# Kernel tuning notes

Hardware: AMD Instinct MI355X
Metric: run time of the kernel (lower is better)

## Reference

```python
import jax, jax.numpy as jnp
import numpy as np

EPS = 1e-5
CONV_CFG = [(10, 5, 3), (8, 5, 2), (4, 2, 1), (3, 1, 1), (3, 1, 1)]  # (kernel, stride, pad)


def conv_bn_relu(x, w, gamma, beta, stride, pad):
    # x: [B, Cin, L], w: [Cout, Cin, K]; BatchNorm1d in training mode (batch stats)
    y = jax.lax.conv_general_dilated(x, w, (stride,), [(pad, pad)],
                                     dimension_numbers=('NCH', 'OIH', 'NCH'))
    mean = y.mean(axis=(0, 2), keepdims=True)
    var = y.var(axis=(0, 2), keepdims=True)
    y = (y - mean) * jax.lax.rsqrt(var + EPS)
    return jax.nn.relu(y * gamma[None, :, None] + beta[None, :, None])


def encoder(x, ws, bn_gamma, bn_beta):
    for i, (k, s, p) in enumerate(CONV_CFG):
        x = conv_bn_relu(x, ws[i], bn_gamma[i], bn_beta[i], s, p)
    return x


def gru(seq, h0, wih, whh, bih, bhh):
    # seq: [B, T, D], h0: [B, H]. torch GRU gate order: r, z, n.
    x_proj = jnp.einsum('btd,gd->btg', seq, wih) + bih  # [B, T, 3H]

    def step(h, xp):
        hp = h @ whh.T + bhh
        xr, xz, xn = jnp.split(xp, 3, axis=-1)
        hr, hz, hn = jnp.split(hp, 3, axis=-1)
        r = jax.nn.sigmoid(xr + hr)
        zg = jax.nn.sigmoid(xz + hz)
        n = jnp.tanh(xn + r * hn)
        h_new = (1.0 - zg) * n + zg * h
        return h_new, h_new

    h_last, outs = jax.lax.scan(step, h0, jnp.swapaxes(x_proj, 0, 1))
    return jnp.swapaxes(outs, 0, 1), h_last


def setup_inputs() -> dict:
    key = jax.random.key(0)
    ks = jax.random.split(key, 16)
    B, L, T = 64, 20480, 12
    x = jax.random.normal(ks[0], (B, 1, L), dtype=jnp.float32)
    hidden = jnp.zeros((1, B, 256), dtype=jnp.float32)
    shapes = [(512, 1, 10), (512, 512, 8), (512, 512, 4), (512, 512, 3), (512, 512, 3)]
    ws = {}
    for i, sh in enumerate(shapes):
        fan_out = sh[0] * sh[2]
        ws['w%d' % (i + 1)] = jax.random.normal(ks[1 + i], sh, dtype=jnp.float32) * np.float32(np.sqrt(2.0 / fan_out))
    bn_gamma = jnp.ones((5, 512), dtype=jnp.float32)
    bn_beta = jnp.zeros((5, 512), dtype=jnp.float32)
    gru_wih = jax.random.normal(ks[6], (768, 512), dtype=jnp.float32) * np.float32(np.sqrt(2.0 / 768.0))
    gru_whh = jax.random.normal(ks[7], (768, 256), dtype=jnp.float32) * np.float32(np.sqrt(2.0 / 768.0))
    gru_bih = jnp.zeros((768,), dtype=jnp.float32)
    gru_bhh = jnp.zeros((768,), dtype=jnp.float32)
    wk_w = jax.random.normal(ks[8], (T, 512, 256), dtype=jnp.float32) * np.float32(np.sqrt(2.0 / 512.0))
    wk_b = jnp.zeros((T, 512), dtype=jnp.float32)
    inp = dict(x=x, hidden=hidden, bn_gamma=bn_gamma, bn_beta=bn_beta,
               gru_wih=gru_wih, gru_whh=gru_whh, gru_bih=gru_bih, gru_bhh=gru_bhh,
               wk_w=wk_w, wk_b=wk_b, t_samples=200)
    inp.update(ws)
    return inp


def reference(x, hidden, w1, w2, w3, w4, w5, bn_gamma, bn_beta,
              gru_wih, gru_whh, gru_bih, gru_bhh, wk_w, wk_b, t_samples):
    B = x.shape[0]
    T = wk_w.shape[0]
    t = int(t_samples)
    z = encoder(x, (w1, w2, w3, w4, w5), bn_gamma, bn_beta)  # [B, 512, Lz]
    z = jnp.swapaxes(z, 1, 2)                                # [B, Lz, 512]
    encode_samples = jnp.swapaxes(z[:, t + 1:t + 1 + T, :], 0, 1)  # [T, B, 512]
    forward_seq = z[:, :t + 1, :]
    output, h_last = gru(forward_seq, hidden[0], gru_wih, gru_whh, gru_bih, gru_bhh)
    c_t = output[:, t, :]                                    # [B, 256]
    pred = jnp.einsum('bd,tkd->tbk', c_t, wk_w) + wk_b[:, None, :]  # [T, B, 512]
    total = jnp.einsum('tbk,tck->tbc', encode_samples, pred)        # [T, B, B]
    logsm = jax.nn.log_softmax(total, axis=-1)  # nn.LogSoftmax() on 2D -> dim=1
    nce = jnp.sum(jnp.diagonal(logsm, axis1=1, axis2=2)) / (-1.0 * B * T)
    # torch overwrites `correct` each iteration -> final value is from the last timestep
    correct = jnp.sum(jnp.argmax(jax.nn.softmax(total[-1], axis=-1), axis=0) == jnp.arange(B))
    accuracy = correct.astype(jnp.float32) / B
    return accuracy, nce, h_last[None]
```

## Files before the change

kernel.cpp:

```cpp
#include <hip/hip_runtime.h>
#include <hip/hip_bf16.h>

typedef __hip_bfloat16 bf16;
typedef short short8v __attribute__((ext_vector_type(8)));
typedef float float4v __attribute__((ext_vector_type(4)));

__device__ __forceinline__ float ld_f(const float* p, size_t i) { return p[i]; }
__device__ __forceinline__ float ld_f(const bf16* p, size_t i) { return __bfloat162float(p[i]); }
__device__ __forceinline__ float bfb_to_f(short u) {
    return __uint_as_float(((unsigned int)(unsigned short)u) << 16);
}
__device__ __forceinline__ short f_to_bf16bits(float v) {
    bf16 h = __float2bfloat16(v);
    short s; __builtin_memcpy(&s, &h, 2); return s;
}
__device__ __forceinline__ unsigned int bn_pair(unsigned int u, float sc, float sh) {
    float x0 = bfb_to_f((short)(u & 0xffffu));
    float x1 = bfb_to_f((short)(u >> 16));
    float y0 = fmaxf(fmaf(sc, x0, sh), 0.0f);
    float y1 = fmaxf(fmaf(sc, x1, sh), 0.0f);
    return (unsigned int)(unsigned short)f_to_bf16bits(y0) |
           ((unsigned int)(unsigned short)f_to_bf16bits(y1) << 16);
}
__device__ __forceinline__ float sigmoidf_(float x) { return 1.0f / (1.0f + expf(-x)); }
// ... 14 lines not shown
    float v = (t < KW) ? w[((size_t)co * CIN + ci) * KW + t] : 0.0f;
    out[idx] = f_to_bf16bits(v);
}

__global__ __launch_bounds__(256) void pack_gruw(const float* __restrict__ whh, short* __restrict__ wfrag) {
    int idx = blockIdx.x * 256 + threadIdx.x;
    if (idx >= 196608) return;
    int j = idx & 7;
    int lane = (idx >> 3) & 63;
    int f = idx >> 9;
    int wv = f / 48;
    int r = f - wv * 48;
    int mt = r >> 3, kc = r & 7;
    int m = lane & 15, quad = lane >> 4;
    int row = (wv * 6 + mt) * 16 + m;
    int col = kc * 32 + quad * 8 + j;
    wfrag[idx] = f_to_bf16bits(whh[(size_t)row * 256 + col]);
}

__global__ __launch_bounds__(256) void pack_all(const float* __restrict__ w3, const float* __restrict__ w4,
                                                const float* __restrict__ w5, const float* __restrict__ wih,
                                                const float* __restrict__ whh,
                                                short* __restrict__ o3, short* __restrict__ o4,
                                                short* __restrict__ o5, short* __restrict__ owih,
                                                short* __restrict__ ogru) {
    int idx = blockIdx.x * 256 + threadIdx.x;
    const int NC = 512 * 512 * 4;
    if (idx < NC) {
        int co = idx >> 11, r = idx & 2047;
        int ci = r >> 2, t = r & 3;
        o3[idx] = f_to_bf16bits(w3[((size_t)co * 512 + ci) * 4 + t]);
        return;
    }
    idx -= NC;
    if (idx < NC) {
        int co = idx >> 11, r = idx & 2047;
        int ci = r >> 2, t = r & 3;
        o4[idx] = (t < 3) ? f_to_bf16bits(w4[((size_t)co * 512 + ci) * 3 + t]) : 0;
        return;
    }
    idx -= NC;
    if (idx < NC) {
        int co = idx >> 11, r = idx & 2047;
        int ci = r >> 2, t = r & 3;
        o5[idx] = (t < 3) ? f_to_bf16bits(w5[((size_t)co * 512 + ci) * 3 + t]) : 0;
        return;
    }
    idx -= NC;
    if (idx < 393216) {
        owih[idx] = f_to_bf16bits(wih[idx]);
        return;
    }
    idx -= 393216;
    if (idx < 196608) {
        int j = idx & 7;
        int lane = (idx >> 3) & 63;
        int f = idx >> 9;
        int wv = f / 48;
        int r = f - wv * 48;
        int mt = r >> 3, kc = r & 7;
        int m = lane & 15, quad = lane >> 4;
        int row = (wv * 6 + mt) * 16 + m;
        int col = kc * 32 + quad * 8 + j;
        ogru[idx] = f_to_bf16bits(whh[(size_t)row * 256 + col]);
    }
}

__global__ __launch_bounds__(256) void bn_fin(const float* __restrict__ sums, const float* __restrict__ gamma,
                                              const float* __restrict__ beta, int layer, float invM,
                                              float* __restrict__ ss) {
    int c = blockIdx.x * 256 + threadIdx.x;
    if (c >= 512) return;
    float mean = sums[c] * invM;
    float var = sums[512 + c] * invM - mean * mean;
    float sc = rsqrtf(var + 1e-5f) * gamma[layer * 512 + c];
    ss[c] = sc;
    ss[512 + c] = beta[layer * 512 + c] - mean * sc;
}

template <int KWP, int ST, int SPANP, bool BNIN, bool STATS>
__global__ __launch_bounds__(256, 3) void conv_mfma6(const bf16* __restrict__ in,
                                                     const short* __restrict__ wpk,
                                                     bf16* __restrict__ out,
                                                     int Lin, int Lout, int pad,
                                                     const float* __restrict__ ssin,
                                                     float* __restrict__ sums_out) {
    constexpr int KTOT = 512 * KWP;
    constexpr int NCHUNK = KTOT / 32;
    constexpr int CCC = 32 / KWP;
    constexpr int W16 = SPANP / 8;
    constexpr int NU = CCC * W16;
    constexpr int NLD = (NU + 255) / 256;

    const int l0 = blockIdx.x * 128;
    const int co0 = blockIdx.y * 128;
    const int tid = threadIdx.x;
    const int lane = tid & 63;
    const int wv = tid >> 6;
    const int m = lane & 15;
    const int quad = lane >> 4;
    const int nh = wv * 32;

    in += (size_t)blockIdx.z * 512 * Lin;
    out += (size_t)blockIdx.z * 512 * Lout;
    const short* ins = (const short*)in;

    __shared__ __align__(16) short As[2][128][40];
    __shared__ __align__(16) short rows[2][CCC][SPANP];
    __shared__ float bsum[STATS ? 128 : 1][2];

    const int base = ST * l0 - pad;
    const int g0a = base & ~7;
    const int off = base - g0a;

    const int arow = tid >> 2, aseg = tid & 3;

    float4v acc[8][2];
#pragma unroll
    for (int i = 0; i < 8; ++i) { acc[i][0] = (float4v){0,0,0,0}; acc[i][1] = (float4v){0,0,0,0}; }

    uint4 pa0, pa1;
    uint4 rbuf[NLD];

    auto load_stage = [&](int kc) {
        const int k0 = kc * 32;
        const int ci0 = kc * CCC;
        pa0 = *(const uint4*)(wpk + (size_t)(co0 + arow) * KTOT + k0 + aseg * 8);
        pa1 = *(const uint4*)(wpk + (size_t)(co0 + arow + 64) * KTOT + k0 + aseg * 8);
#pragma unroll
        for (int r = 0; r < NLD; ++r) {
            int e = tid + r * 256;
            if (NU % 256 == 0 || e < NU) {
                int cc = e / W16, col = e - cc * W16;
                int gs = g0a + col * 8;
                const short* src = ins + (size_t)(ci0 + cc) * Lin;
                if (gs >= 0 && gs + 8 <= Lin) {
                    rbuf[r] = *(const uint4*)(src + gs);
                } else {
                    float sc = 0.f, sh = 0.f;
                    if constexpr (BNIN) { sc = ssin[ci0 + cc]; sh = ssin[512 + ci0 + cc]; }
                    unsigned short tmp[8];
#pragma unroll
                    for (int j = 0; j < 8; ++j) {
                        int g = gs + j;
                        float xv = 0.f;
                        if (g >= 0 && g < Lin) {
                            xv = bfb_to_f(src[g]);
                            if constexpr (BNIN) xv = fmaxf(fmaf(sc, xv, sh), 0.0f);
                        }
                        tmp[j] = (unsigned short)f_to_bf16bits(xv);
                    }
                    uint4 v;
                    v.x = tmp[0] | ((unsigned int)tmp[1] << 16);
                    v.y = tmp[2] | ((unsigned int)tmp[3] << 16);
                    v.z = tmp[4] | ((unsigned int)tmp[5] << 16);
                    v.w = tmp[6] | ((unsigned int)tmp[7] << 16);
                    rbuf[r] = v;
                }
            }
        }
    };
    auto commit = [&](int buf, int kc) {
        *(uint4*)&As[buf][arow][aseg * 8] = pa0;
        *(uint4*)&As[buf][arow + 64][aseg * 8] = pa1;
        const int ci0 = kc * CCC;
#pragma unroll
        for (int r = 0; r < NLD; ++r) {
            int e = tid + r * 256;
            if (NU % 256 == 0 || e < NU) {
                int cc = e / W16, col = e - cc * W16;
                uint4 v = rbuf[r];
                if constexpr (BNIN) {
                    int gs = g0a + col * 8;
                    if (gs >= 0 && gs + 8 <= Lin) {
                        float sc = ssin[ci0 + cc], sh = ssin[512 + ci0 + cc];
                        v.x = bn_pair(v.x, sc, sh);
                        v.y = bn_pair(v.y, sc, sh);
                        v.z = bn_pair(v.z, sc, sh);
                        v.w = bn_pair(v.w, sc, sh);
                    }
                }
                *(uint4*)&rows[buf][cc][col * 8] = v;
            }
        }
    };

    if (STATS && tid < 128) { bsum[tid][0] = 0.f; bsum[tid][1] = 0.f; }
// ... 7 lines not shown

        short8v afrag[8], bfrag[2];
#pragma unroll
        for (int s = 0; s < 8; ++s)
            afrag[s] = *(const short8v*)&As[cur][s * 16 + m][quad * 8];
#pragma unroll
        for (int t = 0; t < 2; ++t) {
            const int ll = nh + t * 16 + m;
            short8v bf;
            if constexpr (KWP == 8) {
                const short* rp = &rows[cur][quad][off + ST * ll];
#pragma unroll
                for (int j = 0; j < 8; ++j) bf[j] = rp[j];
            } else {
                const short* ra = &rows[cur][quad * 2 + 0][off + ST * ll];
                const short* rb = &rows[cur][quad * 2 + 1][off + ST * ll];
#pragma unroll
                for (int j = 0; j < 4; ++j) { bf[j] = ra[j]; bf[4 + j] = rb[j]; }
            }
            bfrag[t] = bf;
        }
#pragma unroll
        for (int s = 0; s < 8; ++s)
#pragma unroll
            for (int t = 0; t < 2; ++t)
                acc[s][t] = __builtin_amdgcn_mfma_f32_16x16x32_bf16(afrag[s], bfrag[t], acc[s][t], 0, 0, 0);

        if (kc + 1 < NCHUNK) commit(cur ^ 1, kc + 1);
        __syncthreads();
    }

    const bool v0 = (l0 + nh + m) < Lout;
    const bool v1 = (l0 + nh + 16 + m) < Lout;
#pragma unroll
    for (int t = 0; t < 2; ++t) {
        const int l = l0 + nh + t * 16 + m;
        if (t ? v1 : v0) {
#pragma unroll
            for (int s = 0; s < 8; ++s) {
#pragma unroll
                for (int reg = 0; reg < 4; ++reg) {
                    const int co = co0 + s * 16 + quad * 4 + reg;
                    out[(size_t)co * Lout + l] = __float2bfloat16(acc[s][t][reg]);
                }
            }
        }
    }

    if constexpr (STATS) {
#pragma unroll
        for (int s = 0; s < 8; ++s) {
            float p1[4], p2[4];
#pragma unroll
            for (int reg = 0; reg < 4; ++reg) {
                float a0 = v0 ? acc[s][0][reg] : 0.f;
                float a1 = v1 ? acc[s][1][reg] : 0.f;
                p1[reg] = a0 + a1;
                p2[reg] = a0 * a0 + a1 * a1;
            }
#pragma unroll
            for (int o = 1; o <= 8; o <<= 1) {
#pragma unroll
                for (int reg = 0; reg < 4; ++reg) {
                    p1[reg] += __shfl_xor(p1[reg], o);
                    p2[reg] += __shfl_xor(p2[reg], o);
                }
            }
            if (m == 0) {
#pragma unroll
                for (int reg = 0; reg < 4; ++reg) {
                    atomicAdd(&bsum[s * 16 + quad * 4 + reg][0], p1[reg]);
                    atomicAdd(&bsum[s * 16 + quad * 4 + reg][1], p2[reg]);
                }
            }
        }
        __syncthreads();
        if (tid < 128) {
            atomicAdd(&sums_out[co0 + tid], bsum[tid][0]);
            atomicAdd(&sums_out[512 + co0 + tid], bsum[tid][1]);
        }
    }
}

__global__ __launch_bounds__(256) void conv1_mfma(const float* __restrict__ x,
                                                  const short* __restrict__ w1p,
                                                  const float* __restrict__ ss,
                                                  bf16* __restrict__ y1c, int nbase) {
    const int l0 = blockIdx.x * 64;
    const int co0 = blockIdx.y * 128;
    const int nloc = blockIdx.z;
    const int n = nbase + nloc;
    const int tid = threadIdx.x;
    const int lane = tid & 63;
    const int wv = tid >> 6;
    const int m = lane & 15;
    const int quad = lane >> 4;

    __shared__ __align__(16) short xs[352];
    const int base = 5 * l0 - 3;
    for (int e = tid; e < 347; e += 256) {
        int g = base + e;
        float v = (g >= 0 && g < 20480) ? x[(size_t)n * 20480 + g] : 0.0f;
        xs[e] = f_to_bf16bits(v);
    }
    __syncthreads();

    const int lloc = wv * 16 + m;
    short8v bfrag;
    {
        const short* rp = &xs[5 * lloc + quad * 8];
#pragma unroll
        for (int j = 0; j < 8; ++j) bfrag[j] = rp[j];
    }
    float4v acc[8];
#pragma unroll
    for (int s = 0; s < 8; ++s) {
        short8v afrag = *(const short8v*)(w1p + (size_t)(co0 + s * 16 + m) * 32 + quad * 8);
        float4v z = (float4v){0.f, 0.f, 0.f, 0.f};
        acc[s] = __builtin_amdgcn_mfma_f32_16x16x32_bf16(afrag, bfrag, z, 0, 0, 0);
    }
    const int l = l0 + lloc;
#pragma unroll
    for (int s = 0; s < 8; ++s) {
#pragma unroll
        for (int reg = 0; reg < 4; ++reg) {
            const int co = co0 + s * 16 + quad * 4 + reg;
            float v = fmaxf(acc[s][reg] * ss[co] + ss[512 + co], 0.0f);
            y1c[((size_t)nloc * 512 + co) * 4096 + l] = __float2bfloat16(v);
        }
    }
}

__global__ __launch_bounds__(256) void conv1_stats(const float* __restrict__ x,
                                                   const float* __restrict__ w1,
                                                   float* __restrict__ sums) {
    const int n = blockIdx.x;
    const int tid = threadIdx.x;
    __shared__ __align__(16) float ws[5120];
    __shared__ __align__(16) float xs[5 * 256 + 10];
    for (int e = tid; e < 5120; e += 256) ws[e] = w1[e];
    const int co0 = tid, co1 = tid + 256;
    float a1_0 = 0.0f, a2_0 = 0.0f, a1_1 = 0.0f, a2_1 = 0.0f;
    for (int i = 0; i < 4; ++i) {
        const int c = blockIdx.y * 4 + i;
        const int base = c * 1280 - 3;
        __syncthreads();
        for (int e = tid; e < 1290; e += 256) {
            int g = base + e;
            xs[e] = (g >= 0 && g < 20480) ? x[(size_t)n * 20480 + g] : 0.0f;
        }
        __syncthreads();
        for (int l = 0; l < 256; ++l) {
            float y0 = 0.0f, y1v = 0.0f;
#pragma unroll
            for (int t = 0; t < 10; ++t) {
                float xv = xs[5 * l + t];
                y0 += ws[co0 * 10 + t] * xv;
                y1v += ws[co1 * 10 + t] * xv;
            }
            a1_0 += y0; a2_0 += y0 * y0;
            a1_1 += y1v; a2_1 += y1v * y1v;
        }
    }
    atomicAdd(&sums[co0], a1_0); atomicAdd(&sums[512 + co0], a2_0);
    atomicAdd(&sums[co1], a1_1); atomicAdd(&sums[512 + co1], a2_1);
}

__global__ __launch_bounds__(256) void bn1_finalize(const float* __restrict__ sums,
                                                    const float* __restrict__ gamma,
                                                    const float* __restrict__ beta,
                                                    float* __restrict__ ss) {
    int c = blockIdx.x * 256 + threadIdx.x;
    if (c >= 512) return;
    const float invM = 1.0f / (64.0f * 4096.0f);
    float mean = sums[c] * invM;
    float var = sums[512 + c] * invM - mean * mean;
    float sc = rsqrtf(var + 1e-5f) * gamma[c];
    ss[c] = sc;
    ss[512 + c] = beta[c] - mean * sc;
}

__global__ __launch_bounds__(256) void bn_stats_v(const bf16* __restrict__ y, float* __restrict__ sums, int L) {
    const int c = blockIdx.x, n = blockIdx.y;
    const short* p = (const short*)y + ((size_t)n * 512 + c) * L;
    float s1 = 0.f, s2 = 0.f;
    for (int l = threadIdx.x; l < L; l += 256) {
        float v = bfb_to_f(p[l]);
        s1 += v; s2 += v * v;
    }
#pragma unroll
    for (int off = 32; off > 0; off >>= 1) {
        s1 += __shfl_down(s1, off, 64);
        s2 += __shfl_down(s2, off, 64);
    }
    __shared__ float r1[4], r2[4];
    const int lane = threadIdx.x & 63, wv = threadIdx.x >> 6;
    if (lane == 0) { r1[wv] = s1; r2[wv] = s2; }
    __syncthreads();
    if (threadIdx.x == 0) {
        atomicAdd(&sums[c], r1[0] + r1[1] + r1[2] + r1[3]);
        atomicAdd(&sums[512 + c], r2[0] + r2[1] + r2[2] + r2[3]);
    }
}

__global__ __launch_bounds__(256) void bn_apply_v(bf16* __restrict__ y, const float* __restrict__ sums,
                                                  const float* __restrict__ gamma, const float* __restrict__ beta,
                                                  int layer, int L) {
    const int c = blockIdx.x, n = blockIdx.y;
    const float invM = 1.0f / (64.0f * (float)L);
    float mean = sums[c] * invM;
    float var = sums[512 + c] * invM - mean * mean;
    float sc = rsqrtf(var + 1e-5f) * gamma[layer * 512 + c];
    float sh = beta[layer * 512 + c] - mean * sc;
    short* p = (short*)y + ((size_t)n * 512 + c) * L;
    for (int l = threadIdx.x; l < L; l += 256) {
        float v = bfb_to_f(p[l]);
        p[l] = f_to_bf16bits(fmaxf(v * sc + sh, 0.0f));
    }
}

__global__ __launch_bounds__(256) void xproj_mfma(const bf16* __restrict__ y5,
                                                  const short* __restrict__ wihp,
                                                  const float* __restrict__ bih,
                                                  float* __restrict__ xp,
                                                  const int* __restrict__ tsamp) {
    const int t0 = blockIdx.x * 64;
    const int g0 = blockIdx.y * 128;
    const int b = blockIdx.z;
    const int tid = threadIdx.x;
    const int lane = tid & 63;
    const int wv = tid >> 6;
    const int m = lane & 15;
    const int quad = lane >> 4;
    const int ts = tsamp[0];

    __shared__ __align__(16) short As[128][40];
    __shared__ __align__(16) short Bt[32][66];

    float4v acc[8];
#pragma unroll
    for (int i = 0; i < 8; ++i) acc[i] = (float4v){0.f, 0.f, 0.f, 0.f};

    const short* y5s = (const short*)y5;
    for (int kc = 0; kc < 16; ++kc) {
        const int k0 = kc * 32;
        __syncthreads();
#pragma unroll
        for (int r = 0; r < 2; ++r) {
            int e = tid + r * 256;
            int row = e >> 2, seg = e & 3;
            *(uint4*)&As[row][seg * 8] =
                *(const uint4*)(wihp + (size_t)(g0 + row) * 512 + k0 + seg * 8);
        }
        for (int e = tid; e < 2048; e += 256) {
            int cc = e >> 6, tl = e & 63;
            Bt[cc][tl] = y5s[((size_t)b * 512 + k0 + cc) * 409 + t0 + tl];
        }
        __syncthreads();
        short8v bfrag;
#pragma unroll
        for (int j = 0; j < 8; ++j) bfrag[j] = Bt[quad * 8 + j][wv * 16 + m];
#pragma unroll
        for (int s = 0; s < 8; ++s) {
            short8v afrag = *(const short8v*)&As[s * 16 + m][quad * 8];
            acc[s] = __builtin_amdgcn_mfma_f32_16x16x32_bf16(afrag, bfrag, acc[s], 0, 0, 0);
        }
    }
    const int t = t0 + wv * 16 + m;
    if (t <= ts) {
#pragma unroll
        for (int s = 0; s < 8; ++s) {
#pragma unroll
            for (int reg = 0; reg < 4; ++reg) {
                const int g = g0 + s * 16 + quad * 4 + reg;
                xp[((size_t)b * 256 + t) * 768 + g] = acc[s][reg] + bih[g];
            }
        }
    }
}

__global__ __launch_bounds__(512, 2) void gru_mfma(const float* __restrict__ xproj,
                                                   const short* __restrict__ wfrag,
                                                   const float* __restrict__ hidden,
                                                   const float* __restrict__ bhh,
                                                   float* __restrict__ hlast,
                                                   const int* __restrict__ tsamp) {
    const int b = blockIdx.x;
    const int tid = threadIdx.x;
    const int lane = tid & 63;
    const int wv = tid >> 6;
    const int m = lane & 15;
    const int quad = lane >> 4;

    __shared__ float hf[256];
    __shared__ __align__(16) short hbs[256];
    __shared__ float pre[768];

    short8v wreg[48];
    {
        const short* wb = wfrag + ((size_t)(wv * 48) * 64 + lane) * 8;
#pragma unroll
        for (int f = 0; f < 48; ++f) wreg[f] = *(const short8v*)(wb + (size_t)f * 512);
    }
    if (wv < 4) {
        float hv = hidden[(size_t)b * 256 + tid];
        hf[tid] = hv;
        hbs[tid] = f_to_bf16bits(hv);
    }
    const int ts = tsamp[0];
    const float* xb = xproj + (size_t)b * 256 * 768;
    float bhr = 0.f, bhz = 0.f, bhn = 0.f, nxr = 0.f, nxz = 0.f, nxn = 0.f;
    if (wv < 4) {
        bhr = bhh[tid]; bhz = bhh[256 + tid]; bhn = bhh[512 + tid];
        nxr = xb[tid]; nxz = xb[256 + tid]; nxn = xb[512 + tid];
    }

    for (int step = 0; step <= ts; ++step) {
        __syncthreads();
        float4v acc[6];
#pragma unroll
        for (int i = 0; i < 6; ++i) acc[i] = (float4v){0.f, 0.f, 0.f, 0.f};
#pragma unroll
        for (int kc = 0; kc < 8; ++kc) {
            short8v bfrag = *(const short8v*)&hbs[kc * 32 + quad * 8];
#pragma unroll
            for (int mt = 0; mt < 6; ++mt)
                acc[mt] = __builtin_amdgcn_mfma_f32_16x16x32_bf16(wreg[mt * 8 + kc], bfrag, acc[mt], 0, 0, 0);
        }
        if (m == 0) {
#pragma unroll
            for (int mt = 0; mt < 6; ++mt)
#pragma unroll
                for (int reg = 0; reg < 4; ++reg)
                    pre[wv * 96 + mt * 16 + quad * 4 + reg] = acc[mt][reg];
        }
        __syncthreads();
        if (wv < 4) {
            const int g = tid;
            float r = sigmoidf_(nxr + bhr + pre[g]);
            float z = sigmoidf_(nxz + bhz + pre[256 + g]);
            float nn = tanhf(nxn + r * (bhn + pre[512 + g]));
            float hnew = (1.0f - z) * nn + z * hf[g];
            hf[g] = hnew;
            hbs[g] = f_to_bf16bits(hnew);
            if (step < ts) {
                const float* xs = xb + (size_t)(step + 1) * 768;
                nxr = xs[g]; nxz = xs[256 + g]; nxn = xs[512 + g];
            }
        }
    }
    __syncthreads();
    if (wv < 4) hlast[(size_t)b * 256 + tid] = hf[tid];
}

__global__ __launch_bounds__(256) void pred_kernel(const float* __restrict__ hlast, const float* __restrict__ wkw,
                                                   const float* __restrict__ wkb, float* __restrict__ pred) {
    const int c = blockIdx.x, t = blockIdx.y;
    __shared__ __align__(16) float hs[256];
    hs[threadIdx.x] = hlast[(size_t)c * 256 + threadIdx.x];
    __syncthreads();
    for (int k = threadIdx.x; k < 512; k += 256) {
        const float* wr = wkw + ((size_t)t * 512 + k) * 256;
        float acc = 0.0f;
        for (int d = 0; d < 256; d += 4) {
            float4 w4 = *(const float4*)&wr[d];
            acc += w4.x * hs[d] + w4.y * hs[d + 1] + w4.z * hs[d + 2] + w4.w * hs[d + 3];
        }
        pred[((size_t)t * 64 + c) * 512 + k] = acc + wkb[(size_t)t * 512 + k];
    }
}

__global__ __launch_bounds__(64) void total_kernel(const bf16* __restrict__ y5, const float* __restrict__ pred,
                                                   float* __restrict__ total, const int* __restrict__ tsamp) {
    const int b = blockIdx.x, t = blockIdx.y;
    const int col = tsamp[0] + 1 + t;
    __shared__ __align__(16) float es[512];
    for (int k = threadIdx.x; k < 512; k += 64) es[k] = ld_f(y5, ((size_t)b * 512 + k) * 409 + col);
    __syncthreads();
    const int c = threadIdx.x;
    const float* pr = pred + ((size_t)t * 64 + c) * 512;
    float acc = 0.0f;
    for (int k = 0; k < 512; k += 4) {
        float4 p4 = *(const float4*)&pr[k];
        acc += p4.x * es[k] + p4.y * es[k + 1] + p4.z * es[k + 2] + p4.w * es[k + 3];
    }
    total[((size_t)t * 64 + b) * 64 + c] = acc;
}

__global__ __launch_bounds__(256) void final_kernel(const float* __restrict__ total, const float* __restrict__ hlast,
                                                    float* __restrict__ out) {
    __shared__ float rowM[768], rowS[768];
    __shared__ float red[256];
    __shared__ int cnt[64];
    const int tid = threadIdx.x;
    float local = 0.0f;
    for (int row = tid; row < 768; row += 256) {
        const float* r = total + (size_t)row * 64;
        float m = r[0];
        for (int c = 1; c < 64; ++c) m = fmaxf(m, r[c]);
        float s = 0.0f;
        for (int c = 0; c < 64; ++c) s += expf(r[c] - m);
        rowM[row] = m; rowS[row] = s;
        int bcol = row & 63;
        local += r[bcol] - m - logf(s);
    }
    red[tid] = local;
    __syncthreads();
    for (int o = 128; o > 0; o >>= 1) {
        if (tid < o) red[tid] += red[tid + o];
        __syncthreads();
    }
    if (tid == 0) out[1] = red[0] / (-768.0f);
    if (tid < 64) {
        const int c = tid;
        float best = -1e30f; int bi = -1;
        for (int b = 0; b < 64; ++b) {
            int row = 11 * 64 + b;
            float v = expf(total[(size_t)row * 64 + c] - rowM[row]) / rowS[row];
            if (v > best) { best = v; bi = b; }
        }
        cnt[c] = (bi == c) ? 1 : 0;
    }
    __syncthreads();
    if (tid == 0) {
        int s = 0;
        for (int c = 0; c < 64; ++c) s += cnt[c];
        out[0] = (float)s / 64.0f;
    }
    for (int i = tid; i < 16384; i += 256) out[2 + i] = hlast[i];
}

extern "C" void kernel_launch(void* const* d_in, const int* in_sizes, int n_in,
                              void* d_out, int out_size, void* d_ws, size_t ws_size,
                              hipStream_t stream) {
    const float *x = nullptr, *hidden = nullptr, *gamma = nullptr, *beta = nullptr;
    const float *wih = nullptr, *whh = nullptr, *bih = nullptr, *bhh = nullptr;
    const float *wkw = nullptr, *wkb = nullptr;
    const float *w1 = nullptr, *w2 = nullptr, *w3 = nullptr, *w4 = nullptr, *w5 = nullptr;
    const int* tsamp = nullptr;
    for (int i = 0; i < n_in; ++i) {
        const float* p = (const float*)d_in[i];
        switch (in_sizes[i]) {
            case 1310720: x = p; break;
            case 16384:   hidden = p; break;
            case 2560:    if (!gamma) gamma = p; else beta = p; break;
            case 393216:  wih = p; break;
            case 196608:  whh = p; break;
            case 768:     if (!bih) bih = p; else bhh = p; break;
            case 1572864: wkw = p; break;
            case 6144:    wkb = p; break;
            case 1:       tsamp = (const int*)d_in[i]; break;
            case 5120:    w1 = p; break;
            case 2097152: w2 = p; break;
            case 1048576: w3 = p; break;
            case 786432:  if (!w4) w4 = p; else w5 = p; break;
            default: break;
        }
    }

    char* ws = (char*)d_ws;
    const size_t SLOT_B = 57872384ull;
    int NBC = 8;
    if (ws_size >= SLOT_B + 64ull * 4194304ull + 81920ull) NBC = 64;
    else if (ws_size >= SLOT_B + 32ull * 4194304ull + 81920ull) NBC = 32;
    else if (ws_size >= SLOT_B + 16ull * 4194304ull + 81920ull) NBC = 16;

    bf16*  y2    = (bf16*)(ws + 0);
    bf16*  y4    = (bf16*)(ws + 0);
    float* xp    = (float*)(ws + 0);
    short* wconv = (short*)(ws + 53676032ull);
    bf16*  y1c   = (bf16*)(ws + SLOT_B);
    bf16*  y3    = (bf16*)(ws + SLOT_B);
    bf16*  y5    = (bf16*)(ws + SLOT_B);
    const size_t tail = SLOT_B + (size_t)NBC * 4194304ull;
    float* sums  = (float*)(ws + tail);
    float* ss1   = (float*)(ws + tail + 20480ull);
    float* ss2   = (float*)(ws + tail + 24576ull);
    float* ss3   = (float*)(ws + tail + 28672ull);
    float* ss4   = (float*)(ws + tail + 32768ull);
    short* w1p   = (short*)(ws + tail + 36864ull);

    float* hlast = (float*)(ws + 54855680ull);
    float* pred  = (float*)(ws + 54921216ull);
    float* totl  = (float*)(ws + 56494080ull);

    short *wpk3, *wpk4, *wpk5, *wihp, *wfrag;
    if (NBC == 64) {
        wpk3  = (short*)(ws + SLOT_B + 33554432ull);
        wpk4  = wpk3 + 1048576;
        wpk5  = wpk4 + 1048576;
        wihp  = wpk5 + 1048576;
        wfrag = wihp + 393216;
    } else {
        wpk3 = wpk4 = wpk5 = wconv;
        wihp  = (short*)(ws + 53676032ull);
        wfrag = (short*)(ws + 54462464ull);
    }

    zero_kernel<<<20, 256, 0, stream>>>(sums, 5120);
    conv1_stats<<<dim3(64, 4), 256, 0, stream>>>(x, w1, sums);
    bn1_finalize<<<2, 256, 0, stream>>>(sums, gamma, beta, ss1);
    pack_gemm<<<64, 256, 0, stream>>>(w1, w1p, 512, 1, 10, 32);
    pack_gemm<<<8192, 256, 0, stream>>>(w2, wconv, 512, 512, 8, 8);

    if (NBC == 64) {
        conv1_mfma<<<dim3(64, 4, 64), 256, 0, stream>>>(x, w1p, ss1, y1c, 0);
        conv_mfma6<8, 5, 656, false, true><<<dim3(7, 4, 64), 256, 0, stream>>>(
            y1c, wconv, y2, 4096, 819, 2, nullptr, sums + 1024);
        pack_all<<<14592, 256, 0, stream>>>(w3, w4, w5, wih, whh, wpk3, wpk4, wpk5, wihp, wfrag);
        bn_fin<<<2, 256, 0, stream>>>(sums + 1024, gamma, beta, 1, 1.0f / (64.0f * 819.0f), ss2);

        conv_mfma6<4, 2, 272, true, true><<<dim3(4, 4, 64), 256, 0, stream>>>(
            y2, wpk3, y3, 819, 409, 1, ss2, sums + 2048);
        bn_fin<<<2, 256, 0, stream>>>(sums + 2048, gamma, beta, 2, 1.0f / (64.0f * 409.0f), ss3);

        conv_mfma6<4, 1, 144, true, true><<<dim3(4, 4, 64), 256, 0, stream>>>(
            y3, wpk4, y4, 409, 409, 1, ss3, sums + 3072);
        bn_fin<<<2, 256, 0, stream>>>(sums + 3072, gamma, beta, 3, 1.0f / (64.0f * 409.0f), ss4);

        conv_mfma6<4, 1, 144, true, true><<<dim3(4, 4, 64), 256, 0, stream>>>(
            y4, wpk5, y5, 409, 409, 1, ss4, sums + 4096);
        bn_apply_v<<<dim3(512, 64), 256, 0, stream>>>(y5, sums + 4096, gamma, beta, 4, 409);
    } else {
        for (int nb = 0; nb < 64; nb += NBC) {
            conv1_mfma<<<dim3(64, 4, NBC), 256, 0, stream>>>(x, w1p, ss1, y1c, nb);
            conv_mfma6<8, 5, 656, false, false><<<dim3(7, 4, NBC), 256, 0, stream>>>(
                y1c, wconv, y2 + (size_t)nb * 512 * 819, 4096, 819, 2, nullptr, nullptr);
        }
        bn_stats_v<<<dim3(512, 64), 256, 0, stream>>>(y2, sums + 1024, 819);
        bn_apply_v<<<dim3(512, 64), 256, 0, stream>>>(y2, sums + 1024, gamma, beta, 1, 819);

        pack_gemm<<<4096, 256, 0, stream>>>(w3, wconv, 512, 512, 4, 4);
        conv_mfma6<4, 2, 272, false, false><<<dim3(4, 4, 64), 256, 0, stream>>>(
            y2, wconv, y3, 819, 409, 1, nullptr, nullptr);
        bn_stats_v<<<dim3(512, 64), 256, 0, stream>>>(y3, sums + 2048, 409);
        bn_apply_v<<<dim3(512, 64), 256, 0, stream>>>(y3, sums + 2048, gamma, beta, 2, 409);

        pack_gemm<<<4096, 256, 0, stream>>>(w4, wconv, 512, 512, 3, 4);
        conv_mfma6<4, 1, 144, false, false><<<dim3(4, 4, 64), 256, 0, stream>>>(
            y3, wconv, y4, 409, 409, 1, nullptr, nullptr);
        bn_stats_v<<<dim3(512, 64), 256, 0, stream>>>(y4, sums + 3072, 409);
        bn_apply_v<<<dim3(512, 64), 256, 0, stream>>>(y4, sums + 3072, gamma, beta, 3, 409);

        pack_gemm<<<4096, 256, 0, stream>>>(w5, wconv, 512, 512, 3, 4);
        conv_mfma6<4, 1, 144, false, false><<<dim3(4, 4, 64), 256, 0, stream>>>(
            y4, wconv, y5, 409, 409, 1, nullptr, nullptr);
        bn_stats_v<<<dim3(512, 64), 256, 0, stream>>>(y5, sums + 4096, 409);
        bn_apply_v<<<dim3(512, 64), 256, 0, stream>>>(y5, sums + 4096, gamma, beta, 4, 409);

        pack_gemm<<<1536, 256, 0, stream>>>(wih, wihp, 768, 512, 1, 1);
        pack_gruw<<<768, 256, 0, stream>>>(whh, wfrag);
    }

    xproj_mfma<<<dim3(4, 6, 64), 256, 0, stream>>>(y5, wihp, bih, xp, tsamp);
    gru_mfma<<<64, 512, 0, stream>>>(xp, wfrag, hidden, bhh, hlast, tsamp);

    pred_kernel<<<dim3(64, 12), 256, 0, stream>>>(hlast, wkw, wkb, pred);
    total_kernel<<<dim3(64, 12), 64, 0, stream>>>(y5, pred, totl, tsamp);
    final_kernel<<<1, 256, 0, stream>>>(totl, hlast, (float*)d_out);
}
```

Measured before the change: 2.120 ms.

## Add full-channel double-buffered conv kernel and fold final BN into consumers

Adds conv_mfma7, where each block covers all 512 output channels for a 64-column tile. It double-buffers the weight and input-row staging through registers and LDS, so each input row is read once rather than by four channel-blocks. Layers 3-5 now use it with a 7x64 grid. The standalone bn_apply pass over y5 is replaced by a small scale/shift finalize that xproj and total_kernel apply on load, removing a full read-modify-write of the activation. Risks: the larger LDS footprint and 128 accumulator registers per thread may limit occupancy, and a stray label was added before a launch.

```diff
diff --git a/kernel.cpp b/kernel.cpp
--- a/kernel.cpp
+++ b/kernel.cpp
@@ -314,6 +314,197 @@
     }
 }
 
+template <int KWP, int ST, int SPANP, bool BNIN, bool STATS>
+__global__ __launch_bounds__(256, 2) void conv_mfma7(const bf16* __restrict__ in,
+                                                     const short* __restrict__ wpk,
+                                                     bf16* __restrict__ out,
+                                                     int Lin, int Lout, int pad,
+                                                     const float* __restrict__ ssin,
+                                                     float* __restrict__ sums_out) {
+    constexpr int KTOT = 512 * KWP;
+    constexpr int NCHUNK = KTOT / 32;
+    constexpr int CCC = 32 / KWP;
+    constexpr int W16 = SPANP / 8;
+    constexpr int NU = CCC * W16;
+
+    const int l0 = blockIdx.x * 64;
+    const int tid = threadIdx.x;
+    const int lane = tid & 63;
+    const int wv = tid >> 6;
+    const int m = lane & 15;
+    const int quad = lane >> 4;
+    const int ch = (wv >> 1) * 256;
+    const int wl = (wv & 1) * 32;
+
+    in += (size_t)blockIdx.y * 512 * Lin;
+    out += (size_t)blockIdx.y * 512 * Lout;
+    const short* ins = (const short*)in;
+
+    __shared__ __align__(16) short As[2][512][32];
+    __shared__ __align__(16) short rows[2][CCC][SPANP];
+    __shared__ float bsum[STATS ? 512 : 1][2];
+
+    const int base = ST * l0 - pad;
+    const int g0a = base & ~7;
+    const int off = base - g0a;
+
+    const int aco = tid >> 2, aseg = tid & 3;
+
+    float4v acc[16][2];
+#pragma unroll
+    for (int i = 0; i < 16; ++i) { acc[i][0] = (float4v){0,0,0,0}; acc[i][1] = (float4v){0,0,0,0}; }
+
+    uint4 pa[8];
+    uint4 rb;
+
+    auto load_stage = [&](int kc) {
+        const int k0 = kc * 32;
+        const int ci0 = kc * CCC;
+#pragma unroll
+        for (int r = 0; r < 8; ++r)
+            pa[r] = *(const uint4*)(wpk + (size_t)(aco + r * 64) * KTOT + k0 + aseg * 8);
+        if (tid < NU) {
+            int cc = tid / W16, col = tid - cc * W16;
+            int gs = g0a + col * 8;
+            const short* src = ins + (size_t)(ci0 + cc) * Lin;
+            if (gs >= 0 && gs + 8 <= Lin) {
+                rb = *(const uint4*)(src + gs);
+            } else {
+                float sc = 0.f, sh = 0.f;
+                if constexpr (BNIN) { sc = ssin[ci0 + cc]; sh = ssin[512 + ci0 + cc]; }
+                unsigned short tmp[8];
+#pragma unroll
+                for (int j = 0; j < 8; ++j) {
+                    int g = gs + j;
+                    float xv = 0.f;
+                    if (g >= 0 && g < Lin) {
+                        xv = bfb_to_f(src[g]);
+                        if constexpr (BNIN) xv = fmaxf(fmaf(sc, xv, sh), 0.0f);
+                    }
+                    tmp[j] = (unsigned short)f_to_bf16bits(xv);
+                }
+                uint4 v;
+                v.x = tmp[0] | ((unsigned int)tmp[1] << 16);
+                v.y = tmp[2] | ((unsigned int)tmp[3] << 16);
+                v.z = tmp[4] | ((unsigned int)tmp[5] << 16);
+                v.w = tmp[6] | ((unsigned int)tmp[7] << 16);
+                rb = v;
+            }
+        }
+    };
+    auto commit = [&](int buf, int kc) {
+#pragma unroll
+        for (int r = 0; r < 8; ++r)
+            *(uint4*)&As[buf][aco + r * 64][aseg * 8] = pa[r];
+        if (tid < NU) {
+            int cc = tid / W16, col = tid - cc * W16;
+            uint4 v = rb;
+            if constexpr (BNIN) {
+                int gs = g0a + col * 8;
+                if (gs >= 0 && gs + 8 <= Lin) {
+                    const int ci0 = kc * CCC;
+                    float sc = ssin[ci0 + cc], sh = ssin[512 + ci0 + cc];
+                    v.x = bn_pair(v.x, sc, sh);
+                    v.y = bn_pair(v.y, sc, sh);
+                    v.z = bn_pair(v.z, sc, sh);
+                    v.w = bn_pair(v.w, sc, sh);
+                }
+            }
+            *(uint4*)&rows[buf][cc][col * 8] = v;
+        }
+    };
+
+    if (STATS) {
+        for (int i = tid; i < 512; i += 256) { bsum[i][0] = 0.f; bsum[i][1] = 0.f; }
+    }
+    load_stage(0);
+    commit(0, 0);
+    __syncthreads();
+
+    for (int kc = 0; kc < NCHUNK; ++kc) {
+        const int cur = kc & 1;
+        if (kc + 1 < NCHUNK) load_stage(kc + 1);
+
+        short8v bfrag[2];
+#pragma unroll
+        for (int t = 0; t < 2; ++t) {
+            const int ll = wl + t * 16 + m;
+            short8v bf;
+            if constexpr (KWP == 8) {
+                const short* rp = &rows[cur][quad][off + ST * ll];
+#pragma unroll
+                for (int j = 0; j < 8; ++j) bf[j] = rp[j];
+            } else {
+                const short* ra = &rows[cur][quad * 2 + 0][off + ST * ll];
+                const short* rb2 = &rows[cur][quad * 2 + 1][off + ST * ll];
+#pragma unroll
+                for (int j = 0; j < 4; ++j) { bf[j] = ra[j]; bf[4 + j] = rb2[j]; }
+            }
+            bfrag[t] = bf;
+        }
+#pragma unroll
+        for (int s = 0; s < 16; ++s) {
+            short8v afrag = *(const short8v*)&As[cur][ch + s * 16 + m][quad * 8];
+            acc[s][0] = __builtin_amdgcn_mfma_f32_16x16x32_bf16(afrag, bfrag[0], acc[s][0], 0, 0, 0);
+            acc[s][1] = __builtin_amdgcn_mfma_f32_16x16x32_bf16(afrag, bfrag[1], acc[s][1], 0, 0, 0);
+        }
+
+        if (kc + 1 < NCHUNK) commit(cur ^ 1, kc + 1);
+        __syncthreads();
+    }
+
+    const bool v0 = (l0 + wl + m) < Lout;
+    const bool v1 = (l0 + wl + 16 + m) < Lout;
+#pragma unroll
+    for (int t = 0; t < 2; ++t) {
+        const int l = l0 + wl + t * 16 + m;
+        if (t ? v1 : v0) {
+#pragma unroll
+            for (int s = 0; s < 16; ++s) {
+#pragma unroll
+                for (int reg = 0; reg < 4; ++reg) {
+                    const int co = ch + s * 16 + quad * 4 + reg;
+                    out[(size_t)co * Lout + l] = __float2bfloat16(acc[s][t][reg]);
+                }
+            }
+        }
+    }
+
+    if constexpr (STATS) {
+#pragma unroll
+        for (int s = 0; s < 16; ++s) {
+            float p1[4], p2[4];
+#pragma unroll
+            for (int reg = 0; reg < 4; ++reg) {
+                float a0 = v0 ? acc[s][0][reg] : 0.f;
+                float a1 = v1 ? acc[s][1][reg] : 0.f;
+                p1[reg] = a0 + a1;
+                p2[reg] = a0 * a0 + a1 * a1;
+            }
+#pragma unroll
+            for (int o = 1; o <= 8; o <<= 1) {
+#pragma unroll
+                for (int reg = 0; reg < 4; ++reg) {
+                    p1[reg] += __shfl_xor(p1[reg], o);
+                    p2[reg] += __shfl_xor(p2[reg], o);
+                }
+            }
+            if (m == 0) {
+#pragma unroll
+                for (int reg = 0; reg < 4; ++reg) {
+                    atomicAdd(&bsum[ch + s * 16 + quad * 4 + reg][0], p1[reg]);
+                    atomicAdd(&bsum[ch + s * 16 + quad * 4 + reg][1], p2[reg]);
+                }
+            }
+        }
+        __syncthreads();
+        for (int i = tid; i < 512; i += 256) {
+            atomicAdd(&sums_out[i], bsum[i][0]);
+            atomicAdd(&sums_out[512 + i], bsum[i][1]);
+        }
+    }
+}
+
 __global__ __launch_bounds__(256) void conv1_mfma(const float* __restrict__ x,
                                                   const short* __restrict__ w1p,
                                                   const float* __restrict__ ss,
@@ -398,20 +589,6 @@
     atomicAdd(&sums[co1], a1_1); atomicAdd(&sums[512 + co1], a2_1);
 }
 
-__global__ __launch_bounds__(256) void bn1_finalize(const float* __restrict__ sums,
-                                                    const float* __restrict__ gamma,
-                                                    const float* __restrict__ beta,
-                                                    float* __restrict__ ss) {
-    int c = blockIdx.x * 256 + threadIdx.x;
-    if (c >= 512) return;
-    const float invM = 1.0f / (64.0f * 4096.0f);
-    float mean = sums[c] * invM;
-    float var = sums[512 + c] * invM - mean * mean;
-    float sc = rsqrtf(var + 1e-5f) * gamma[c];
-    ss[c] = sc;
-    ss[512 + c] = beta[c] - mean * sc;
-}
-
 __global__ __launch_bounds__(256) void bn_stats_v(const bf16* __restrict__ y, float* __restrict__ sums, int L) {
     const int c = blockIdx.x, n = blockIdx.y;
     const short* p = (const short*)y + ((size_t)n * 512 + c) * L;
@@ -454,6 +631,7 @@
 __global__ __launch_bounds__(256) void xproj_mfma(const bf16* __restrict__ y5,
                                                   const short* __restrict__ wihp,
                                                   const float* __restrict__ bih,
+                                                  const float* __restrict__ ssy,
                                                   float* __restrict__ xp,
                                                   const int* __restrict__ tsamp) {
     const int t0 = blockIdx.x * 64;
@@ -486,7 +664,9 @@
         }
         for (int e = tid; e < 2048; e += 256) {
             int cc = e >> 6, tl = e & 63;
-            Bt[cc][tl] = y5s[((size_t)b * 512 + k0 + cc) * 409 + t0 + tl];
+            float sc = ssy[k0 + cc], sh = ssy[512 + k0 + cc];
+            float xv = bfb_to_f(y5s[((size_t)b * 512 + k0 + cc) * 409 + t0 + tl]);
+            Bt[cc][tl] = f_to_bf16bits(fmaxf(fmaf(sc, xv, sh), 0.0f));
         }
         __syncthreads();
         short8v bfrag;
@@ -603,11 +783,15 @@
 }
 
 __global__ __launch_bounds__(64) void total_kernel(const bf16* __restrict__ y5, const float* __restrict__ pred,
+                                                   const float* __restrict__ ssy,
                                                    float* __restrict__ total, const int* __restrict__ tsamp) {
     const int b = blockIdx.x, t = blockIdx.y;
     const int col = tsamp[0] + 1 + t;
     __shared__ __align__(16) float es[512];
-    for (int k = threadIdx.x; k < 512; k += 64) es[k] = ld_f(y5, ((size_t)b * 512 + k) * 409 + col);
+    for (int k = threadIdx.x; k < 512; k += 64) {
+        float xv = ld_f(y5, ((size_t)b * 512 + k) * 409 + col);
+        es[k] = fmaxf(fmaf(ssy[k], xv, ssy[512 + k]), 0.0f);
+    }
     __syncthreads();
     const int c = threadIdx.x;
     const float* pr = pred + ((size_t)t * 64 + c) * 512;
@@ -693,9 +877,9 @@
     char* ws = (char*)d_ws;
     const size_t SLOT_B = 57872384ull;
     int NBC = 8;
-    if (ws_size >= SLOT_B + 64ull * 4194304ull + 81920ull) NBC = 64;
-    else if (ws_size >= SLOT_B + 32ull * 4194304ull + 81920ull) NBC = 32;
-    else if (ws_size >= SLOT_B + 16ull * 4194304ull + 81920ull) NBC = 16;
+    if (ws_size >= SLOT_B + 64ull * 4194304ull + 98304ull) NBC = 64;
+    else if (ws_size >= SLOT_B + 32ull * 4194304ull + 98304ull) NBC = 32;
+    else if (ws_size >= SLOT_B + 16ull * 4194304ull + 98304ull) NBC = 16;
 
     bf16*  y2    = (bf16*)(ws + 0);
     bf16*  y4    = (bf16*)(ws + 0);
@@ -710,7 +894,8 @@
     float* ss2   = (float*)(ws + tail + 24576ull);
     float* ss3   = (float*)(ws + tail + 28672ull);
     float* ss4   = (float*)(ws + tail + 32768ull);
-    short* w1p   = (short*)(ws + tail + 36864ull);
+    float* ss5   = (float*)(ws + tail + 36864ull);
+    short* w1p   = (short*)(ws + tail + 40960ull);
 
     float* hlast = (float*)(ws + 54855680ull);
     float* pred  = (float*)(ws + 54921216ull);
@@ -731,7 +916,8 @@
 
     zero_kernel<<<20, 256, 0, stream>>>(sums, 5120);
     conv1_stats<<<dim3(64, 4), 256, 0, stream>>>(x, w1, sums);
-    bn1_finalize<<<2, 256, 0, stream>>>(sums, gamma, beta, ss1);
+    bn1_finalize_launch:
+    bn_fin<<<2, 256, 0, stream>>>(sums, gamma, beta, 0, 1.0f / (64.0f * 4096.0f), ss1);
     pack_gemm<<<64, 256, 0, stream>>>(w1, w1p, 512, 1, 10, 32);
     pack_gemm<<<8192, 256, 0, stream>>>(w2, wconv, 512, 512, 8, 8);
 
@@ -742,17 +928,17 @@
         pack_all<<<14592, 256, 0, stream>>>(w3, w4, w5, wih, whh, wpk3, wpk4, wpk5, wihp, wfrag);
         bn_fin<<<2, 256, 0, stream>>>(sums + 1024, gamma, beta, 1, 1.0f / (64.0f * 819.0f), ss2);
 
-        conv_mfma6<4, 2, 272, true, true><<<dim3(4, 4, 64), 256, 0, stream>>>(
+        conv_mfma7<4, 2, 144, true, true><<<dim3(7, 64), 256, 0, stream>>>(
             y2, wpk3, y3, 819, 409, 1, ss2, sums + 2048);
         bn_fin<<<2, 256, 0, stream>>>(sums + 2048, gamma, beta, 2, 1.0f / (64.0f * 409.0f), ss3);
 
-        conv_mfma6<4, 1, 144, true, true><<<dim3(4, 4, 64), 256, 0, stream>>>(
+        conv_mfma7<4, 1, 80, true, true><<<dim3(7, 64), 256, 0, stream>>>(
             y3, wpk4, y4, 409, 409, 1, ss3, sums + 3072);
         bn_fin<<<2, 256, 0, stream>>>(sums + 3072, gamma, beta, 3, 1.0f / (64.0f * 409.0f), ss4);
 
-        conv_mfma6<4, 1, 144, true, true><<<dim3(4, 4, 64), 256, 0, stream>>>(
+        conv_mfma7<4, 1, 80, true, true><<<dim3(7, 64), 256, 0, stream>>>(
             y4, wpk5, y5, 409, 409, 1, ss4, sums + 4096);
-        bn_apply_v<<<dim3(512, 64), 256, 0, stream>>>(y5, sums + 4096, gamma, beta, 4, 409);
+        bn_fin<<<2, 256, 0, stream>>>(sums + 4096, gamma, beta, 4, 1.0f / (64.0f * 409.0f), ss5);
     } else {
         for (int nb = 0; nb < 64; nb += NBC) {
             conv1_mfma<<<dim3(64, 4, NBC), 256, 0, stream>>>(x, w1p, ss1, y1c, nb);
@@ -763,31 +949,31 @@
         bn_apply_v<<<dim3(512, 64), 256, 0, stream>>>(y2, sums + 1024, gamma, beta, 1, 819);
 
         pack_gemm<<<4096, 256, 0, stream>>>(w3, wconv, 512, 512, 4, 4);
-        conv_mfma6<4, 2, 272, false, false><<<dim3(4, 4, 64), 256, 0, stream>>>(
+        conv_mfma7<4, 2, 144, false, false><<<dim3(7, 64), 256, 0, stream>>>(
             y2, wconv, y3, 819, 409, 1, nullptr, nullptr);
         bn_stats_v<<<dim3(512, 64), 256, 0, stream>>>(y3, sums + 2048, 409);
         bn_apply_v<<<dim3(512, 64), 256, 0, stream>>>(y3, sums + 2048, gamma, beta, 2, 409);
 
         pack_gemm<<<4096, 256, 0, stream>>>(w4, wconv, 512, 512, 3, 4);
-        conv_mfma6<4, 1, 144, false, false><<<dim3(4, 4, 64), 256, 0, stream>>>(
+        conv_mfma7<4, 1, 80, false, false><<<dim3(7, 64), 256, 0, stream>>>(
             y3, wconv, y4, 409, 409, 1, nullptr, nullptr);
         bn_stats_v<<<dim3(512, 64), 256, 0, stream>>>(y4, sums + 3072, 409);
         bn_apply_v<<<dim3(512, 64), 256, 0, stream>>>(y4, sums + 3072, gamma, beta, 3, 409);
 
         pack_gemm<<<4096, 256, 0, stream>>>(w5, wconv, 512, 512, 3, 4);
-        conv_mfma6<4, 1, 144, false, false><<<dim3(4, 4, 64), 256, 0, stream>>>(
+        conv_mfma7<4, 1, 80, false, false><<<dim3(7, 64), 256, 0, stream>>>(
             y4, wconv, y5, 409, 409, 1, nullptr, nullptr);
         bn_stats_v<<<dim3(512, 64), 256, 0, stream>>>(y5, sums + 4096, 409);
-        bn_apply_v<<<dim3(512, 64), 256, 0, stream>>>(y5, sums + 4096, gamma, beta, 4, 409);
+        bn_fin<<<2, 256, 0, stream>>>(sums + 4096, gamma, beta, 4, 1.0f / (64.0f * 409.0f), ss5);
 
         pack_gemm<<<1536, 256, 0, stream>>>(wih, wihp, 768, 512, 1, 1);
         pack_gruw<<<768, 256, 0, stream>>>(whh, wfrag);
     }
 
-    xproj_mfma<<<dim3(4, 6, 64), 256, 0, stream>>>(y5, wihp, bih, xp, tsamp);
+    xproj_mfma<<<dim3(4, 6, 64), 256, 0, stream>>>(y5, wihp, bih, ss5, xp, tsamp);
     gru_mfma<<<64, 512, 0, stream>>>(xp, wfrag, hidden, bhh, hlast, tsamp);
 
     pred_kernel<<<dim3(64, 12), 256, 0, stream>>>(hlast, wkw, wkb, pred);
-    total_kernel<<<dim3(64, 12), 64, 0, stream>>>(y5, pred, totl, tsamp);
+    total_kernel<<<dim3(64, 12), 64, 0, stream>>>(y5, pred, ss5, totl, tsamp);
     final_kernel<<<1, 256, 0, stream>>>(totl, hlast, (float*)d_out);
 }
```

New measurement: 2.528 ms. 1.19x slower.

## Fold final BN into consumers and swizzle conv block order for L2 reuse

Applied to the files above, without the earlier changes.

Drops the standalone bn_apply pass over y5 and instead computes scale/shift with bn_fin, applying BN+ReLU on the fly in xproj_mfma and total_kernel loads. This removes a full read-modify-write pass over the last activation tensor. Conv blocks now use a 1D grid remapped so that groups of 8 length tiles cycle through all 4 output-channel tiles consecutively, aiming for better cache reuse of input tiles. It also changes the workspace layout to add an ss5 slot.

```diff
diff --git a/kernel.cpp b/kernel.cpp
--- a/kernel.cpp
+++ b/kernel.cpp
@@ -120,7 +120,7 @@
 __global__ __launch_bounds__(256, 3) void conv_mfma6(const bf16* __restrict__ in,
                                                      const short* __restrict__ wpk,
                                                      bf16* __restrict__ out,
-                                                     int Lin, int Lout, int pad,
+                                                     int Lin, int Lout, int pad, int NL,
                                                      const float* __restrict__ ssin,
                                                      float* __restrict__ sums_out) {
     constexpr int KTOT = 512 * KWP;
@@ -130,8 +130,14 @@
     constexpr int NU = CCC * W16;
     constexpr int NLD = (NU + 255) / 256;
 
-    const int l0 = blockIdx.x * 128;
-    const int co0 = blockIdx.y * 128;
+    const int lin = blockIdx.x;
+    const int co_t = (lin >> 3) & 3;
+    const int u = ((lin >> 5) << 3) | (lin & 7);
+    const int l_t = u % NL;
+    const int n = u / NL;
+    const int l0 = l_t * 128;
+    const int co0 = co_t * 128;
+
     const int tid = threadIdx.x;
     const int lane = tid & 63;
     const int wv = tid >> 6;
@@ -139,8 +145,8 @@
     const int quad = lane >> 4;
     const int nh = wv * 32;
 
-    in += (size_t)blockIdx.z * 512 * Lin;
-    out += (size_t)blockIdx.z * 512 * Lout;
+    in += (size_t)n * 512 * Lin;
+    out += (size_t)n * 512 * Lout;
     const short* ins = (const short*)in;
 
     __shared__ __align__(16) short As[2][128][40];
@@ -398,20 +404,6 @@
     atomicAdd(&sums[co1], a1_1); atomicAdd(&sums[512 + co1], a2_1);
 }
 
-__global__ __launch_bounds__(256) void bn1_finalize(const float* __restrict__ sums,
-                                                    const float* __restrict__ gamma,
-                                                    const float* __restrict__ beta,
-                                                    float* __restrict__ ss) {
-    int c = blockIdx.x * 256 + threadIdx.x;
-    if (c >= 512) return;
-    const float invM = 1.0f / (64.0f * 4096.0f);
-    float mean = sums[c] * invM;
-    float var = sums[512 + c] * invM - mean * mean;
-    float sc = rsqrtf(var + 1e-5f) * gamma[c];
-    ss[c] = sc;
-    ss[512 + c] = beta[c] - mean * sc;
-}
-
 __global__ __launch_bounds__(256) void bn_stats_v(const bf16* __restrict__ y, float* __restrict__ sums, int L) {
     const int c = blockIdx.x, n = blockIdx.y;
     const short* p = (const short*)y + ((size_t)n * 512 + c) * L;
@@ -454,6 +446,7 @@
 __global__ __launch_bounds__(256) void xproj_mfma(const bf16* __restrict__ y5,
                                                   const short* __restrict__ wihp,
                                                   const float* __restrict__ bih,
+                                                  const float* __restrict__ ssy,
                                                   float* __restrict__ xp,
                                                   const int* __restrict__ tsamp) {
     const int t0 = blockIdx.x * 64;
@@ -486,7 +479,9 @@
         }
         for (int e = tid; e < 2048; e += 256) {
             int cc = e >> 6, tl = e & 63;
-            Bt[cc][tl] = y5s[((size_t)b * 512 + k0 + cc) * 409 + t0 + tl];
+            float sc = ssy[k0 + cc], sh = ssy[512 + k0 + cc];
+            float xv = bfb_to_f(y5s[((size_t)b * 512 + k0 + cc) * 409 + t0 + tl]);
+            Bt[cc][tl] = f_to_bf16bits(fmaxf(fmaf(sc, xv, sh), 0.0f));
         }
         __syncthreads();
         short8v bfrag;
@@ -603,11 +598,15 @@
 }
 
 __global__ __launch_bounds__(64) void total_kernel(const bf16* __restrict__ y5, const float* __restrict__ pred,
+                                                   const float* __restrict__ ssy,
                                                    float* __restrict__ total, const int* __restrict__ tsamp) {
     const int b = blockIdx.x, t = blockIdx.y;
     const int col = tsamp[0] + 1 + t;
     __shared__ __align__(16) float es[512];
-    for (int k = threadIdx.x; k < 512; k += 64) es[k] = ld_f(y5, ((size_t)b * 512 + k) * 409 + col);
+    for (int k = threadIdx.x; k < 512; k += 64) {
+        float xv = ld_f(y5, ((size_t)b * 512 + k) * 409 + col);
+        es[k] = fmaxf(fmaf(ssy[k], xv, ssy[512 + k]), 0.0f);
+    }
     __syncthreads();
     const int c = threadIdx.x;
     const float* pr = pred + ((size_t)t * 64 + c) * 512;
@@ -693,9 +692,9 @@
     char* ws = (char*)d_ws;
     const size_t SLOT_B = 57872384ull;
     int NBC = 8;
-    if (ws_size >= SLOT_B + 64ull * 4194304ull + 81920ull) NBC = 64;
-    else if (ws_size >= SLOT_B + 32ull * 4194304ull + 81920ull) NBC = 32;
-    else if (ws_size >= SLOT_B + 16ull * 4194304ull + 81920ull) NBC = 16;
+    if (ws_size >= SLOT_B + 64ull * 4194304ull + 98304ull) NBC = 64;
+    else if (ws_size >= SLOT_B + 32ull * 4194304ull + 98304ull) NBC = 32;
+    else if (ws_size >= SLOT_B + 16ull * 4194304ull + 98304ull) NBC = 16;
 
     bf16*  y2    = (bf16*)(ws + 0);
     bf16*  y4    = (bf16*)(ws + 0);
@@ -710,7 +709,8 @@
     float* ss2   = (float*)(ws + tail + 24576ull);
     float* ss3   = (float*)(ws + tail + 28672ull);
     float* ss4   = (float*)(ws + tail + 32768ull);
-    short* w1p   = (short*)(ws + tail + 36864ull);
+    float* ss5   = (float*)(ws + tail + 36864ull);
+    short* w1p   = (short*)(ws + tail + 40960ull);
 
     float* hlast = (float*)(ws + 54855680ull);
     float* pred  = (float*)(ws + 54921216ull);
@@ -731,63 +731,63 @@
 
     zero_kernel<<<20, 256, 0, stream>>>(sums, 5120);
     conv1_stats<<<dim3(64, 4), 256, 0, stream>>>(x, w1, sums);
-    bn1_finalize<<<2, 256, 0, stream>>>(sums, gamma, beta, ss1);
+    bn_fin<<<2, 256, 0, stream>>>(sums, gamma, beta, 0, 1.0f / (64.0f * 4096.0f), ss1);
     pack_gemm<<<64, 256, 0, stream>>>(w1, w1p, 512, 1, 10, 32);
     pack_gemm<<<8192, 256, 0, stream>>>(w2, wconv, 512, 512, 8, 8);
 
     if (NBC == 64) {
         conv1_mfma<<<dim3(64, 4, 64), 256, 0, stream>>>(x, w1p, ss1, y1c, 0);
-        conv_mfma6<8, 5, 656, false, true><<<dim3(7, 4, 64), 256, 0, stream>>>(
-            y1c, wconv, y2, 4096, 819, 2, nullptr, sums + 1024);
+        conv_mfma6<8, 5, 656, false, true><<<7 * 4 * 64, 256, 0, stream>>>(
+            y1c, wconv, y2, 4096, 819, 2, 7, nullptr, sums + 1024);
         pack_all<<<14592, 256, 0, stream>>>(w3, w4, w5, wih, whh, wpk3, wpk4, wpk5, wihp, wfrag);
         bn_fin<<<2, 256, 0, stream>>>(sums + 1024, gamma, beta, 1, 1.0f / (64.0f * 819.0f), ss2);
 
-        conv_mfma6<4, 2, 272, true, true><<<dim3(4, 4, 64), 256, 0, stream>>>(
-            y2, wpk3, y3, 819, 409, 1, ss2, sums + 2048);
+        conv_mfma6<4, 2, 272, true, true><<<4 * 4 * 64, 256, 0, stream>>>(
+            y2, wpk3, y3, 819, 409, 1, 4, ss2, sums + 2048);
         bn_fin<<<2, 256, 0, stream>>>(sums + 2048, gamma, beta, 2, 1.0f / (64.0f * 409.0f), ss3);
 
-        conv_mfma6<4, 1, 144, true, true><<<dim3(4, 4, 64), 256, 0, stream>>>(
-            y3, wpk4, y4, 409, 409, 1, ss3, sums + 3072);
+        conv_mfma6<4, 1, 144, true, true><<<4 * 4 * 64, 256, 0, stream>>>(
+            y3, wpk4, y4, 409, 409, 1, 4, ss3, sums + 3072);
         bn_fin<<<2, 256, 0, stream>>>(sums + 3072, gamma, beta, 3, 1.0f / (64.0f * 409.0f), ss4);
 
-        conv_mfma6<4, 1, 144, true, true><<<dim3(4, 4, 64), 256, 0, stream>>>(
-            y4, wpk5, y5, 409, 409, 1, ss4, sums + 4096);
-        bn_apply_v<<<dim3(512, 64), 256, 0, stream>>>(y5, sums + 4096, gamma, beta, 4, 409);
+        conv_mfma6<4, 1, 144, true, true><<<4 * 4 * 64, 256, 0, stream>>>(
+            y4, wpk5, y5, 409, 409, 1, 4, ss4, sums + 4096);
+        bn_fin<<<2, 256, 0, stream>>>(sums + 4096, gamma, beta, 4, 1.0f / (64.0f * 409.0f), ss5);
     } else {
         for (int nb = 0; nb < 64; nb += NBC) {
             conv1_mfma<<<dim3(64, 4, NBC), 256, 0, stream>>>(x, w1p, ss1, y1c, nb);
-            conv_mfma6<8, 5, 656, false, false><<<dim3(7, 4, NBC), 256, 0, stream>>>(
-                y1c, wconv, y2 + (size_t)nb * 512 * 819, 4096, 819, 2, nullptr, nullptr);
+            conv_mfma6<8, 5, 656, false, false><<<7 * 4 * NBC, 256, 0, stream>>>(
+                y1c, wconv, y2 + (size_t)nb * 512 * 819, 4096, 819, 2, 7, nullptr, nullptr);
         }
         bn_stats_v<<<dim3(512, 64), 256, 0, stream>>>(y2, sums + 1024, 819);
         bn_apply_v<<<dim3(512, 64), 256, 0, stream>>>(y2, sums + 1024, gamma, beta, 1, 819);
 
         pack_gemm<<<4096, 256, 0, stream>>>(w3, wconv, 512, 512, 4, 4);
-        conv_mfma6<4, 2, 272, false, false><<<dim3(4, 4, 64), 256, 0, stream>>>(
-            y2, wconv, y3, 819, 409, 1, nullptr, nullptr);
+        conv_mfma6<4, 2, 272, false, false><<<4 * 4 * 64, 256, 0, stream>>>(
+            y2, wconv, y3, 819, 409, 1, 4, nullptr, nullptr);
         bn_stats_v<<<dim3(512, 64), 256, 0, stream>>>(y3, sums + 2048, 409);
         bn_apply_v<<<dim3(512, 64), 256, 0, stream>>>(y3, sums + 2048, gamma, beta, 2, 409);
 
         pack_gemm<<<4096, 256, 0, stream>>>(w4, wconv, 512, 512, 3, 4);
-        conv_mfma6<4, 1, 144, false, false><<<dim3(4, 4, 64), 256, 0, stream>>>(
-            y3, wconv, y4, 409, 409, 1, nullptr, nullptr);
+        conv_mfma6<4, 1, 144, false, false><<<4 * 4 * 64, 256, 0, stream>>>(
+            y3, wconv, y4, 409, 409, 1, 4, nullptr, nullptr);
         bn_stats_v<<<dim3(512, 64), 256, 0, stream>>>(y4, sums + 3072, 409);
         bn_apply_v<<<dim3(512, 64), 256, 0, stream>>>(y4, sums + 3072, gamma, beta, 3, 409);
 
         pack_gemm<<<4096, 256, 0, stream>>>(w5, wconv, 512, 512, 3, 4);
-        conv_mfma6<4, 1, 144, false, false><<<dim3(4, 4, 64), 256, 0, stream>>>(
-            y4, wconv, y5, 409, 409, 1, nullptr, nullptr);
+        conv_mfma6<4, 1, 144, false, false><<<4 * 4 * 64, 256, 0, stream>>>(
+            y4, wconv, y5, 409, 409, 1, 4, nullptr, nullptr);
         bn_stats_v<<<dim3(512, 64), 256, 0, stream>>>(y5, sums + 4096, 409);
-        bn_apply_v<<<dim3(512, 64), 256, 0, stream>>>(y5, sums + 4096, gamma, beta, 4, 409);
+        bn_fin<<<2, 256, 0, stream>>>(sums + 4096, gamma, beta, 4, 1.0f / (64.0f * 409.0f), ss5);
 
         pack_gemm<<<1536, 256, 0, stream>>>(wih, wihp, 768, 512, 1, 1);
         pack_gruw<<<768, 256, 0, stream>>>(whh, wfrag);
     }
 
-    xproj_mfma<<<dim3(4, 6, 64), 256, 0, stream>>>(y5, wihp, bih, xp, tsamp);
+    xproj_mfma<<<dim3(4, 6, 64), 256, 0, stream>>>(y5, wihp, bih, ss5, xp, tsamp);
     gru_mfma<<<64, 512, 0, stream>>>(xp, wfrag, hidden, bhh, hlast, tsamp);
 
     pred_kernel<<<dim3(64, 12), 256, 0, stream>>>(hlast, wkw, wkb, pred);
-    total_kernel<<<dim3(64, 12), 64, 0, stream>>>(y5, pred, totl, tsamp);
+    total_kernel<<<dim3(64, 12), 64, 0, stream>>>(y5, pred, ss5, totl, tsamp);
     final_kernel<<<1, 256, 0, stream>>>(totl, hlast, (float*)d_out);
 }
```

Result: no change. 2.086 ms (-1.6%).
